# Kernel tuning notes

Measured on AMD Instinct MI355X. Metric: run time of the kernel, lower is better.

The kernel has to match this reference:

```python
import jax, jax.numpy as jnp
import numpy as np

N_NODES = 50000
N_EDGES = 800000


def _gcn_conv(x, src, dst, norm, W, b, num_nodes):
    # x: [N, Fin] -> h: [N, Fout]; messages gathered from src, scattered to dst.
    h = x @ W
    msgs = h[src] * norm[:, None]                      # [E+N, Fout]
    out = jax.ops.segment_sum(msgs, dst, num_segments=num_nodes)
    return out + b


def _gcn_norm(edge_index, num_nodes):
    # Add self-loops and compute symmetric normalization D^-1/2 (A+I) D^-1/2.
    loops = jnp.arange(num_nodes, dtype=edge_index.dtype)
    src = jnp.concatenate([edge_index[0], loops])
    dst = jnp.concatenate([edge_index[1], loops])
    ones = jnp.ones(src.shape[0], dtype=jnp.float32)
    deg = jax.ops.segment_sum(ones, dst, num_segments=num_nodes)
    dinv = jnp.where(deg > 0, jax.lax.rsqrt(jnp.maximum(deg, 1.0)), 0.0)
    norm = dinv[src] * dinv[dst]
    return src, dst, norm


def setup_inputs() -> dict:
    key = jax.random.key(0)
    k1, k2, k3, k4 = jax.random.split(key, 4)
    map_x = jax.random.normal(k1, (N_NODES, 128), dtype=jnp.float32)
    edge_index = jax.random.randint(k2, (2, N_EDGES), 0, N_NODES, dtype=jnp.int64)
    W1 = jax.random.normal(k3, (128, 64), dtype=jnp.float32) * (1.0 / np.sqrt(128))
    b1 = jnp.zeros((64,), dtype=jnp.float32)
    W2 = jax.random.normal(k4, (64, 32), dtype=jnp.float32) * (1.0 / np.sqrt(64))
    b2 = jnp.zeros((32,), dtype=jnp.float32)
    return {"map": map_x, "edge_index": edge_index, "W1": W1, "b1": b1, "W2": W2, "b2": b2}


def reference(map, edge_index, W1, b1, W2, b2):
    num_nodes = map.shape[0]
    src, dst, norm = _gcn_norm(edge_index, num_nodes)
    x = jax.nn.relu(_gcn_conv(map, src, dst, norm, W1, b1, num_nodes))
    x = jax.nn.relu(_gcn_conv(x, src, dst, norm, W2, b2, num_nodes))
    return x
```

## Files before the change

kernel.cpp:

```cpp
#include <hip/hip_runtime.h>

#define TPB 256
#define ACHUNK 4096
#define BSHIFT 6
#define BNODES 64
#define CAP 2048

__device__ __forceinline__ float blo(unsigned u) { return __uint_as_float(u << 16); }
__device__ __forceinline__ float bhi(unsigned u) { return __uint_as_float(u & 0xffff0000u); }
__device__ __forceinline__ unsigned pack2(float a, float b) {
    unsigned ua = __float_as_uint(a); ua += 0x7fffu + ((ua >> 16) & 1u);
    unsigned ub = __float_as_uint(b); ub += 0x7fffu + ((ub >> 16) & 1u);
    return (ua >> 16) | (ub & 0xffff0000u);
}
__device__ __forceinline__ void dec8(uint4 v, float* f) {
    f[0] = blo(v.x); f[1] = bhi(v.x); f[2] = blo(v.y); f[3] = bhi(v.y);
    f[4] = blo(v.z); f[5] = bhi(v.z); f[6] = blo(v.w); f[7] = bhi(v.w);
}
__device__ __forceinline__ void dec4(uint2 v, float* f) {
    f[0] = blo(v.x); f[1] = bhi(v.x); f[2] = blo(v.y); f[3] = bhi(v.y);
}


__global__ __launch_bounds__(TPB) void k_fat(
        const int* __restrict__ src, const int* __restrict__ dst, int E,
        int* __restrict__ bcnt, int* __restrict__ tmp, int NB,
        const float* __restrict__ X, const float* __restrict__ W,
        unsigned int* __restrict__ H1b, int N, int G1, int FB) {
    __shared__ float Ws[128 * 64];
    int* lcnt = (int*)Ws;
    int bid = blockIdx.x;
    int t = threadIdx.x;

    if ((bid % 5) == 0) {
        int fidx = bid / 5;
        if (fidx >= FB) return;
        int c0 = fidx * ACHUNK;
        int s_[16], d_[16];
#pragma unroll
        for (int i = 0; i < 16; i++) {
            int e = c0 + i * TPB + t;
            if (e < E) { s_[i] = src[e]; d_[i] = dst[e]; }
            else d_[i] = -1;
        }
        for (int b = t; b < NB; b += TPB) lcnt[b] = 0;
        __syncthreads();
#pragma unroll
        for (int i = 0; i < 16; i++)
            if (d_[i] >= 0) atomicAdd(&lcnt[d_[i] >> BSHIFT], 1);
        __syncthreads();
        for (int b = t; b < NB; b += TPB) {
            int c = lcnt[b];
            lcnt[b] = c ? (b * CAP + atomicAdd(&bcnt[b], c)) : 0;
        }
        __syncthreads();
#pragma unroll
        for (int i = 0; i < 16; i++) {
            if (d_[i] >= 0) {
                int bkt = d_[i] >> BSHIFT;
                int pos = atomicAdd(&lcnt[bkt], 1);
                if (pos < (bkt + 1) * CAP) {
                    tmp[pos] = ((d_[i] & (BNODES - 1)) << 16) | s_[i];
                }
            }
        }
    } else {
        int gb = bid - bid / 5 - 1;
        if (gb >= G1) return;
        int row0 = gb * 64;

        const float4* W4 = (const float4*)W;
        float4* Ws4 = (float4*)Ws;
#pragma unroll
        for (int i = 0; i < 8; i++) Ws4[t + i * 256] = W4[t + i * 256];
        __syncthreads();

        int r = t >> 2;
        int c0 = (t & 3) * 16;
        if (row0 + r >= N) return;
        const float4* xr = (const float4*)(X + (size_t)(row0 + r) * 128);
        float acc[16];
#pragma unroll
        for (int j = 0; j < 16; j++) acc[j] = 0.0f;
        for (int kk = 0; kk < 32; kk++) {
            float4 xv = xr[kk];
            const float* w0 = Ws + (4 * kk) * 64 + c0;
#pragma unroll
            for (int j = 0; j < 16; j++) acc[j] = fmaf(xv.x, w0[j], acc[j]);
#pragma unroll
            for (int j = 0; j < 16; j++) acc[j] = fmaf(xv.y, w0[64 + j], acc[j]);
#pragma unroll
            for (int j = 0; j < 16; j++) acc[j] = fmaf(xv.z, w0[128 + j], acc[j]);
#pragma unroll
            for (int j = 0; j < 16; j++) acc[j] = fmaf(xv.w, w0[192 + j], acc[j]);
        }
        unsigned int* ho = H1b + (size_t)(row0 + r) * 32 + (t & 3) * 8;
        uint4 p0 = { pack2(acc[0], acc[1]), pack2(acc[2], acc[3]),
                     pack2(acc[4], acc[5]), pack2(acc[6], acc[7]) };
        uint4 p1 = { pack2(acc[8], acc[9]), pack2(acc[10], acc[11]),
                     pack2(acc[12], acc[13]), pack2(acc[14], acc[15]) };
        *(uint4*)ho = p0;
        *(uint4*)(ho + 4) = p1;
    }
}


__global__ __launch_bounds__(TPB) void k_binB(
        const int* __restrict__ bcnt, const int* __restrict__ tmp,
        int* __restrict__ rowptr, unsigned short* __restrict__ rowlen,
        float* __restrict__ dinv, unsigned short* __restrict__ edges,
        unsigned short* __restrict__ order,
        const unsigned int* __restrict__ H1b, unsigned int* __restrict__ g1b,
        int N) {
    __shared__ int hist[BNODES];
    __shared__ int cur[BNODES];
    __shared__ int sh[BNODES];
    __shared__ int db[BNODES];
    __shared__ float dl[BNODES];
    int b = blockIdx.x;
    int t = threadIdx.x;
    int node0 = b << BSHIFT;
    int nn = N - node0; if (nn > BNODES) nn = BNODES;
    int cnt = bcnt[b]; if (cnt > CAP) cnt = CAP;
    const int tb = b * CAP;

    if (t < BNODES) hist[t] = 0;
    __syncthreads();
    for (int i = t; i < cnt; i += TPB) atomicAdd(&hist[tmp[tb + i] >> 16], 1);
    __syncthreads();
    if (t < BNODES) sh[t] = hist[t];
    __syncthreads();
    for (int o = 1; o < BNODES; o <<= 1) {
        int x = (t >= o && t < BNODES) ? sh[t - o] : 0;
        __syncthreads();
        if (t < BNODES) sh[t] += x;
        __syncthreads();
    }
    int v = 0;
    if (t < BNODES) {
        v = hist[t];
        int excl = sh[t] - v;
        cur[t] = excl;
        float dv = rsqrtf((float)(v + 1));
        dl[t] = dv;
        if (t < nn) {
            dinv[node0 + t] = dv;
            rowptr[node0 + t] = tb + excl;
            rowlen[node0 + t] = (unsigned short)v;
        }
    }
    int dcap = v > 63 ? 63 : v;
    if (t < BNODES) db[t] = 0;
    __syncthreads();
    if (t < nn) atomicAdd(&db[dcap], 1);
    __syncthreads();
    int dc = (t < BNODES) ? db[t] : 0;
    if (t < BNODES) sh[t] = dc;
    __syncthreads();
    for (int o = 1; o < BNODES; o <<= 1) {
        int x = (t >= o && t < BNODES) ? sh[t - o] : 0;
        __syncthreads();
        if (t < BNODES) sh[t] += x;
        __syncthreads();
    }
    if (t < BNODES) db[t] = sh[t] - dc;
    __syncthreads();
    if (t < nn) {
        int pos = atomicAdd(&db[dcap], 1);
        order[node0 + pos] = (unsigned short)(node0 + t);
    }
    __syncthreads();
    for (int i = t; i < cnt; i += TPB) {
        int p = tmp[tb + i];
        int pos = atomicAdd(&cur[p >> 16], 1);
        edges[tb + pos] = (unsigned short)(p & 0xffff);
    }
    const uint4* H4 = (const uint4*)H1b;
    uint4* G4 = (uint4*)g1b;
    for (int i = t; i < nn * 8; i += TPB) {
        int r = i >> 3, q = i & 7;
        float dv = dl[r];
        float f[8];
        uint4 hv = H4[(size_t)(node0 + r) * 8 + q];
        dec8(hv, f);
        uint4 p = { pack2(f[0] * dv, f[1] * dv), pack2(f[2] * dv, f[3] * dv),
                    pack2(f[4] * dv, f[5] * dv), pack2(f[6] * dv, f[7] * dv) };
        G4[(size_t)(node0 + r) * 8 + q] = p;
    }
}


__global__ __launch_bounds__(TPB) void k_gg(
        const int* __restrict__ rowptr, const unsigned short* __restrict__ rowlen,
        const unsigned short* __restrict__ edges, const unsigned short* __restrict__ order,
        const unsigned int* __restrict__ g1b,
        const float* __restrict__ dinv, const float* __restrict__ b1,
        const float* __restrict__ W2, unsigned int* __restrict__ g2b, int N) {
    __shared__ float W2s[64 * 32];
    __shared__ float rows[32 * 68];
    __shared__ float dl[32];
    __shared__ int nid[32];
    __shared__ int nst[32];
    __shared__ int nlen[32];
    int t = threadIdx.x;
    int node0 = blockIdx.x * 32;
    int nn = N - node0; if (nn > 32) nn = 32;
    if (nn <= 0) return;

    {
        const float4* W4 = (const float4*)W2;
        float4* Wd = (float4*)W2s;
        Wd[t] = W4[t]; Wd[t + 256] = W4[t + 256];
    }
    if (t < nn) {
        int ord = order[node0 + t];
        nid[t] = ord;
        dl[t] = dinv[ord];
        nst[t] = rowptr[ord];
        nlen[t] = rowlen[ord];
    }
    __syncthreads();

    const uint4* G4 = (const uint4*)g1b;
    int nl = t >> 3;
    int lane = t & 7;
    if (nl < nn) {
        int ord = nid[nl];
        float acc[8], f[8];
        uint4 sv = G4[(size_t)ord * 8 + lane];
        dec8(sv, acc);
        int base = nst[nl], deg = nlen[nl];
        int j = 0;
        for (; j + 7 < deg; j += 8) {
            int s0 = edges[base + j],     s1 = edges[base + j + 1];
            int s2 = edges[base + j + 2], s3 = edges[base + j + 3];
            int s4 = edges[base + j + 4], s5 = edges[base + j + 5];
            int s6 = edges[base + j + 6], s7 = edges[base + j + 7];
            uint4 r0 = G4[(size_t)s0 * 8 + lane];
            uint4 r1 = G4[(size_t)s1 * 8 + lane];
            uint4 r2 = G4[(size_t)s2 * 8 + lane];
            uint4 r3 = G4[(size_t)s3 * 8 + lane];
            uint4 r4 = G4[(size_t)s4 * 8 + lane];
            uint4 r5 = G4[(size_t)s5 * 8 + lane];
            uint4 r6 = G4[(size_t)s6 * 8 + lane];
            uint4 r7 = G4[(size_t)s7 * 8 + lane];
            dec8(r0, f);
#pragma unroll
            for (int k = 0; k < 8; k++) acc[k] += f[k];
            dec8(r1, f);
#pragma unroll
            for (int k = 0; k < 8; k++) acc[k] += f[k];
            dec8(r2, f);
#pragma unroll
            for (int k = 0; k < 8; k++) acc[k] += f[k];
            dec8(r3, f);
#pragma unroll
            for (int k = 0; k < 8; k++) acc[k] += f[k];
            dec8(r4, f);
#pragma unroll
            for (int k = 0; k < 8; k++) acc[k] += f[k];
            dec8(r5, f);
#pragma unroll
            for (int k = 0; k < 8; k++) acc[k] += f[k];
            dec8(r6, f);
#pragma unroll
            for (int k = 0; k < 8; k++) acc[k] += f[k];
            dec8(r7, f);
#pragma unroll
            for (int k = 0; k < 8; k++) acc[k] += f[k];
        }
        for (; j < deg; j++) {
            int s0 = edges[base + j];
            uint4 r0 = G4[(size_t)s0 * 8 + lane];
            dec8(r0, f);
#pragma unroll
            for (int k = 0; k < 8; k++) acc[k] += f[k];
        }
        float w0 = dl[nl];
        const float4* bb4 = (const float4*)(b1 + lane * 8);
        float4 ba = bb4[0], bc = bb4[1];
        float* rr = rows + nl * 68 + lane * 8;
        rr[0] = fmaxf(fmaf(acc[0], w0, ba.x), 0.0f);
        rr[1] = fmaxf(fmaf(acc[1], w0, ba.y), 0.0f);
        rr[2] = fmaxf(fmaf(acc[2], w0, ba.z), 0.0f);
        rr[3] = fmaxf(fmaf(acc[3], w0, ba.w), 0.0f);
        rr[4] = fmaxf(fmaf(acc[4], w0, bc.x), 0.0f);
        rr[5] = fmaxf(fmaf(acc[5], w0, bc.y), 0.0f);
        rr[6] = fmaxf(fmaf(acc[6], w0, bc.z), 0.0f);
        rr[7] = fmaxf(fmaf(acc[7], w0, bc.w), 0.0f);
    }
    __syncthreads();

    int n = t >> 3;
    int c = t & 7;
    if (n < nn) {
        const float* row = rows + n * 68;
        float a0 = 0.0f, a1 = 0.0f, a2 = 0.0f, a3 = 0.0f;
#pragma unroll 8
        for (int k = 0; k < 64; k++) {
            float rv = row[k];
            const float* w = W2s + k * 32 + 4 * c;
            a0 = fmaf(rv, w[0], a0); a1 = fmaf(rv, w[1], a1);
            a2 = fmaf(rv, w[2], a2); a3 = fmaf(rv, w[3], a3);
        }
        float dv = dl[n];
        uint2 p = { pack2(a0 * dv, a1 * dv), pack2(a2 * dv, a3 * dv) };
        ((uint2*)g2b)[(size_t)nid[n] * 8 + c] = p;
    }
}


__global__ __launch_bounds__(TPB) void k_g32(
        const int* __restrict__ rowptr, const unsigned short* __restrict__ rowlen,
        const unsigned short* __restrict__ edges, const unsigned short* __restrict__ order,
        const unsigned int* __restrict__ g2b,
        const float* __restrict__ dinv, const float* __restrict__ b2,
        float* __restrict__ out, int N) {
    __shared__ float dl[32];
    __shared__ int nid[32];
    __shared__ int nst[32];
    __shared__ int nlen[32];
    int t = threadIdx.x;
    int node0 = blockIdx.x * 32;
    int nn = N - node0; if (nn > 32) nn = 32;
    if (nn <= 0) return;
    if (t < nn) {
        int ord = order[node0 + t];
        nid[t] = ord;
        dl[t] = dinv[ord];
        nst[t] = rowptr[ord];
        nlen[t] = rowlen[ord];
    }
    __syncthreads();

    int nl = t >> 3;
    int lane = t & 7;
    if (nl >= nn) return;

    const uint2* G2 = (const uint2*)g2b;
    int ord = nid[nl];
    float acc[4], f[4];
    uint2 sv = G2[(size_t)ord * 8 + lane];
    dec4(sv, acc);
    int base = nst[nl], deg = nlen[nl];
    int j = 0;
    for (; j + 7 < deg; j += 8) {
        int s0 = edges[base + j],     s1 = edges[base + j + 1];
        int s2 = edges[base + j + 2], s3 = edges[base + j + 3];
        int s4 = edges[base + j + 4], s5 = edges[base + j + 5];
        int s6 = edges[base + j + 6], s7 = edges[base + j + 7];
        uint2 r0 = G2[(size_t)s0 * 8 + lane];
        uint2 r1 = G2[(size_t)s1 * 8 + lane];
        uint2 r2 = G2[(size_t)s2 * 8 + lane];
        uint2 r3 = G2[(size_t)s3 * 8 + lane];
        uint2 r4 = G2[(size_t)s4 * 8 + lane];
        uint2 r5 = G2[(size_t)s5 * 8 + lane];
        uint2 r6 = G2[(size_t)s6 * 8 + lane];
        uint2 r7 = G2[(size_t)s7 * 8 + lane];
        dec4(r0, f); acc[0] += f[0]; acc[1] += f[1]; acc[2] += f[2]; acc[3] += f[3];
        dec4(r1, f); acc[0] += f[0]; acc[1] += f[1]; acc[2] += f[2]; acc[3] += f[3];
        dec4(r2, f); acc[0] += f[0]; acc[1] += f[1]; acc[2] += f[2]; acc[3] += f[3];
        dec4(r3, f); acc[0] += f[0]; acc[1] += f[1]; acc[2] += f[2]; acc[3] += f[3];
        dec4(r4, f); acc[0] += f[0]; acc[1] += f[1]; acc[2] += f[2]; acc[3] += f[3];
        dec4(r5, f); acc[0] += f[0]; acc[1] += f[1]; acc[2] += f[2]; acc[3] += f[3];
        dec4(r6, f); acc[0] += f[0]; acc[1] += f[1]; acc[2] += f[2]; acc[3] += f[3];
        dec4(r7, f); acc[0] += f[0]; acc[1] += f[1]; acc[2] += f[2]; acc[3] += f[3];
    }
    for (; j < deg; j++) {
        int s0 = edges[base + j];
        uint2 r0 = G2[(size_t)s0 * 8 + lane];
        dec4(r0, f); acc[0] += f[0]; acc[1] += f[1]; acc[2] += f[2]; acc[3] += f[3];
    }
    float w0 = dl[nl];
    const float4* bb4 = (const float4*)(b2 + lane * 4);
    float4 ba = bb4[0];
    float4 o0 = { fmaxf(fmaf(acc[0], w0, ba.x), 0.0f),
                  fmaxf(fmaf(acc[1], w0, ba.y), 0.0f),
                  fmaxf(fmaf(acc[2], w0, ba.z), 0.0f),
                  fmaxf(fmaf(acc[3], w0, ba.w), 0.0f) };
    *(float4*)(out + (size_t)ord * 32 + lane * 4) = o0;
}

static inline int cdiv(int a, int b) { return (a + b - 1) / b; }
static inline char* alignup(char* p) { return (char*)(((uintptr_t)p + 255) & ~(uintptr_t)255); }

extern "C" void kernel_launch(void* const* d_in, const int* in_sizes, int n_in,
                              void* d_out, int out_size, void* d_ws, size_t ws_size,
                              hipStream_t stream) {
    const float* x  = (const float*)d_in[0];
    const int*   ei = (const int*)d_in[1];
    const float* W1 = (const float*)d_in[2];
    const float* b1 = (const float*)d_in[3];
    const float* W2 = (const float*)d_in[4];
    const float* b2 = (const float*)d_in[5];
    float* out = (float*)d_out;

    int N = in_sizes[0] / 128;
    int E = in_sizes[1] / 2;
    const int* src = ei;
    const int* dst = ei + E;

    int NB = cdiv(N, BNODES);

    char* p = (char*)d_ws;
    float* dinv  = (float*)p;            p = alignup(p + sizeof(float) * N);
    int* rowptr  = (int*)p;              p = alignup(p + sizeof(int) * N);
    unsigned short* rowlen = (unsigned short*)p;  p = alignup(p + sizeof(short) * N);
    unsigned short* order  = (unsigned short*)p;  p = alignup(p + sizeof(short) * N);
    int* bcnt    = (int*)p;              p = alignup(p + sizeof(int) * 1024);
    int* tmp     = (int*)p;              p = alignup(p + sizeof(int) * (size_t)NB * CAP);
    unsigned short* edges = (unsigned short*)p;   p = alignup(p + sizeof(short) * (size_t)NB * CAP);
    unsigned int* h1b = (unsigned int*)p; p = alignup(p + sizeof(short) * (size_t)N * 64);
    unsigned int* g1b = (unsigned int*)p; p = alignup(p + sizeof(short) * (size_t)N * 64);
    unsigned int* g2b = (unsigned int*)p; p = alignup(p + sizeof(short) * (size_t)N * 32);

    dim3 blk(TPB);
    int FB = cdiv(E, ACHUNK);
    int G1 = cdiv(N, 64);
    int fat = 1;
    while ((fat + 4) / 5 < FB || fat - (fat + 4) / 5 < G1) fat++;

    hipMemsetAsync(bcnt, 0, sizeof(int) * 1024, stream);
    k_fat<<<fat, blk, 0, stream>>>(src, dst, E, bcnt, tmp, NB,
                                   x, W1, h1b, N, G1, FB);
    k_binB<<<NB, blk, 0, stream>>>(bcnt, tmp, rowptr, rowlen, dinv,
                                   edges, order, h1b, g1b, N);
    k_gg<<<cdiv(N, 32), blk, 0, stream>>>(rowptr, rowlen, edges, order, g1b,
                                          dinv, b1, W2, g2b, N);
    k_g32<<<cdiv(N, 32), blk, 0, stream>>>(rowptr, rowlen, edges, order, g2b,
                                           dinv, b2, out, N);
}
```

Measured before the change: 154.5 us.

## Register-tile first GEMM, drop degree-sorted node order, widen gather unroll

The first-layer GEMM in the fused kernel now has each thread compute a 4-row by 8-column register tile over 128 rows per block, reusing shared-memory weight loads across rows. The block interleave ratio changes from 1:4 to 1:2. The per-bucket degree-sort that produced a node order permutation is removed, so the aggregation kernels process nodes in natural order and skip the indirection. The second-layer gather loop is unrolled to 16 outstanding loads. Dropping the sort removes a scan and extra syncs in the binning kernel, but gives up degree-balanced wavefronts in the gather kernels.

Measured after the change: 151.4 us (median of 3 runs). -2.0%, faster.

```diff
diff --git a/kernel.cpp b/kernel.cpp
--- a/kernel.cpp
+++ b/kernel.cpp
@@ -5,6 +5,7 @@
 #define BSHIFT 6
 #define BNODES 64
 #define CAP 2048
+#define GROWS 128
 
 __device__ __forceinline__ float blo(unsigned u) { return __uint_as_float(u << 16); }
 __device__ __forceinline__ float bhi(unsigned u) { return __uint_as_float(u & 0xffff0000u); }
@@ -32,8 +33,8 @@
     int bid = blockIdx.x;
     int t = threadIdx.x;
 
-    if ((bid % 5) == 0) {
-        int fidx = bid / 5;
+    if ((bid % 3) == 0) {
+        int fidx = bid / 3;
         if (fidx >= FB) return;
         int c0 = fidx * ACHUNK;
         int s_[16], d_[16];
@@ -65,9 +66,9 @@
             }
         }
     } else {
-        int gb = bid - bid / 5 - 1;
+        int gb = bid - bid / 3 - 1;
         if (gb >= G1) return;
-        int row0 = gb * 64;
+        int row0 = gb * GROWS;
 
         const float4* W4 = (const float4*)W;
         float4* Ws4 = (float4*)Ws;
@@ -75,32 +76,50 @@
         for (int i = 0; i < 8; i++) Ws4[t + i * 256] = W4[t + i * 256];
         __syncthreads();
 
-        int r = t >> 2;
-        int c0 = (t & 3) * 16;
-        if (row0 + r >= N) return;
-        const float4* xr = (const float4*)(X + (size_t)(row0 + r) * 128);
-        float acc[16];
-#pragma unroll
-        for (int j = 0; j < 16; j++) acc[j] = 0.0f;
+        int rg = t >> 3;
+        int c0 = (t & 7) * 8;
+        int r0 = row0 + rg * 4;
+        int ri[4];
+#pragma unroll
+        for (int i = 0; i < 4; i++) ri[i] = (r0 + i < N) ? (r0 + i) : (N - 1);
+
+        float acc[4][8];
+#pragma unroll
+        for (int i = 0; i < 4; i++)
+#pragma unroll
+            for (int j = 0; j < 8; j++) acc[i][j] = 0.0f;
+
+        const float4* X4 = (const float4*)X;
         for (int kk = 0; kk < 32; kk++) {
-            float4 xv = xr[kk];
-            const float* w0 = Ws + (4 * kk) * 64 + c0;
-#pragma unroll
-            for (int j = 0; j < 16; j++) acc[j] = fmaf(xv.x, w0[j], acc[j]);
-#pragma unroll
-            for (int j = 0; j < 16; j++) acc[j] = fmaf(xv.y, w0[64 + j], acc[j]);
-#pragma unroll
-            for (int j = 0; j < 16; j++) acc[j] = fmaf(xv.z, w0[128 + j], acc[j]);
-#pragma unroll
-            for (int j = 0; j < 16; j++) acc[j] = fmaf(xv.w, w0[192 + j], acc[j]);
-        }
-        unsigned int* ho = H1b + (size_t)(row0 + r) * 32 + (t & 3) * 8;
-        uint4 p0 = { pack2(acc[0], acc[1]), pack2(acc[2], acc[3]),
-                     pack2(acc[4], acc[5]), pack2(acc[6], acc[7]) };
-        uint4 p1 = { pack2(acc[8], acc[9]), pack2(acc[10], acc[11]),
-                     pack2(acc[12], acc[13]), pack2(acc[14], acc[15]) };
-        *(uint4*)ho = p0;
-        *(uint4*)(ho + 4) = p1;
+            float4 xv[4];
+#pragma unroll
+            for (int i = 0; i < 4; i++) xv[i] = X4[(size_t)ri[i] * 32 + kk];
+#pragma unroll
+            for (int q = 0; q < 4; q++) {
+                const float* w = Ws + (4 * kk + q) * 64 + c0;
+                float wq[8];
+#pragma unroll
+                for (int j = 0; j < 8; j++) wq[j] = w[j];
+                float xq[4];
+                xq[0] = q == 0 ? xv[0].x : q == 1 ? xv[0].y : q == 2 ? xv[0].z : xv[0].w;
+                xq[1] = q == 0 ? xv[1].x : q == 1 ? xv[1].y : q == 2 ? xv[1].z : xv[1].w;
+                xq[2] = q == 0 ? xv[2].x : q == 1 ? xv[2].y : q == 2 ? xv[2].z : xv[2].w;
+                xq[3] = q == 0 ? xv[3].x : q == 1 ? xv[3].y : q == 2 ? xv[3].z : xv[3].w;
+#pragma unroll
+                for (int i = 0; i < 4; i++)
+#pragma unroll
+                    for (int j = 0; j < 8; j++)
+                        acc[i][j] = fmaf(xq[i], wq[j], acc[i][j]);
+            }
+        }
+#pragma unroll
+        for (int i = 0; i < 4; i++) {
+            if (r0 + i < N) {
+                uint4 p = { pack2(acc[i][0], acc[i][1]), pack2(acc[i][2], acc[i][3]),
+                            pack2(acc[i][4], acc[i][5]), pack2(acc[i][6], acc[i][7]) };
+                *(uint4*)(H1b + (size_t)(r0 + i) * 32 + (t & 7) * 4) = p;
+            }
+        }
     }
 }
 
@@ -109,13 +128,11 @@
         const int* __restrict__ bcnt, const int* __restrict__ tmp,
         int* __restrict__ rowptr, unsigned short* __restrict__ rowlen,
         float* __restrict__ dinv, unsigned short* __restrict__ edges,
-        unsigned short* __restrict__ order,
         const unsigned int* __restrict__ H1b, unsigned int* __restrict__ g1b,
         int N) {
     __shared__ int hist[BNODES];
     __shared__ int cur[BNODES];
     __shared__ int sh[BNODES];
-    __shared__ int db[BNODES];
     __shared__ float dl[BNODES];
     int b = blockIdx.x;
     int t = threadIdx.x;
@@ -136,9 +153,8 @@
         if (t < BNODES) sh[t] += x;
         __syncthreads();
     }
-    int v = 0;
     if (t < BNODES) {
-        v = hist[t];
+        int v = hist[t];
         int excl = sh[t] - v;
         cur[t] = excl;
         float dv = rsqrtf((float)(v + 1));
@@ -148,26 +164,6 @@
             rowptr[node0 + t] = tb + excl;
             rowlen[node0 + t] = (unsigned short)v;
         }
-    }
-    int dcap = v > 63 ? 63 : v;
-    if (t < BNODES) db[t] = 0;
-    __syncthreads();
-    if (t < nn) atomicAdd(&db[dcap], 1);
-    __syncthreads();
-    int dc = (t < BNODES) ? db[t] : 0;
-    if (t < BNODES) sh[t] = dc;
-    __syncthreads();
-    for (int o = 1; o < BNODES; o <<= 1) {
-        int x = (t >= o && t < BNODES) ? sh[t - o] : 0;
-        __syncthreads();
-        if (t < BNODES) sh[t] += x;
-        __syncthreads();
-    }
-    if (t < BNODES) db[t] = sh[t] - dc;
-    __syncthreads();
-    if (t < nn) {
-        int pos = atomicAdd(&db[dcap], 1);
-        order[node0 + pos] = (unsigned short)(node0 + t);
     }
     __syncthreads();
     for (int i = t; i < cnt; i += TPB) {
@@ -192,14 +188,13 @@
 
 __global__ __launch_bounds__(TPB) void k_gg(
         const int* __restrict__ rowptr, const unsigned short* __restrict__ rowlen,
-        const unsigned short* __restrict__ edges, const unsigned short* __restrict__ order,
+        const unsigned short* __restrict__ edges,
         const unsigned int* __restrict__ g1b,
         const float* __restrict__ dinv, const float* __restrict__ b1,
         const float* __restrict__ W2, unsigned int* __restrict__ g2b, int N) {
     __shared__ float W2s[64 * 32];
     __shared__ float rows[32 * 68];
     __shared__ float dl[32];
-    __shared__ int nid[32];
     __shared__ int nst[32];
     __shared__ int nlen[32];
     int t = threadIdx.x;
@@ -213,11 +208,9 @@
         Wd[t] = W4[t]; Wd[t + 256] = W4[t + 256];
     }
     if (t < nn) {
-        int ord = order[node0 + t];
-        nid[t] = ord;
-        dl[t] = dinv[ord];
-        nst[t] = rowptr[ord];
-        nlen[t] = rowlen[ord];
+        dl[t] = dinv[node0 + t];
+        nst[t] = rowptr[node0 + t];
+        nlen[t] = rowlen[node0 + t];
     }
     __syncthreads();
 
@@ -225,53 +218,25 @@
     int nl = t >> 3;
     int lane = t & 7;
     if (nl < nn) {
-        int ord = nid[nl];
         float acc[8], f[8];
-        uint4 sv = G4[(size_t)ord * 8 + lane];
+        uint4 sv = G4[(size_t)(node0 + nl) * 8 + lane];
         dec8(sv, acc);
         int base = nst[nl], deg = nlen[nl];
         int j = 0;
         for (; j + 7 < deg; j += 8) {
-            int s0 = edges[base + j],     s1 = edges[base + j + 1];
-            int s2 = edges[base + j + 2], s3 = edges[base + j + 3];
-            int s4 = edges[base + j + 4], s5 = edges[base + j + 5];
-            int s6 = edges[base + j + 6], s7 = edges[base + j + 7];
-            uint4 r0 = G4[(size_t)s0 * 8 + lane];
-            uint4 r1 = G4[(size_t)s1 * 8 + lane];
-            uint4 r2 = G4[(size_t)s2 * 8 + lane];
-            uint4 r3 = G4[(size_t)s3 * 8 + lane];
-            uint4 r4 = G4[(size_t)s4 * 8 + lane];
-            uint4 r5 = G4[(size_t)s5 * 8 + lane];
-            uint4 r6 = G4[(size_t)s6 * 8 + lane];
-            uint4 r7 = G4[(size_t)s7 * 8 + lane];
-            dec8(r0, f);
-#pragma unroll
-            for (int k = 0; k < 8; k++) acc[k] += f[k];
-            dec8(r1, f);
-#pragma unroll
-            for (int k = 0; k < 8; k++) acc[k] += f[k];
-            dec8(r2, f);
-#pragma unroll
-            for (int k = 0; k < 8; k++) acc[k] += f[k];
-            dec8(r3, f);
-#pragma unroll
-            for (int k = 0; k < 8; k++) acc[k] += f[k];
-            dec8(r4, f);
-#pragma unroll
-            for (int k = 0; k < 8; k++) acc[k] += f[k];
-            dec8(r5, f);
-#pragma unroll
-            for (int k = 0; k < 8; k++) acc[k] += f[k];
-            dec8(r6, f);
-#pragma unroll
-            for (int k = 0; k < 8; k++) acc[k] += f[k];
-            dec8(r7, f);
-#pragma unroll
-            for (int k = 0; k < 8; k++) acc[k] += f[k];
+            uint4 r[8];
+#pragma unroll
+            for (int u = 0; u < 8; u++)
+                r[u] = G4[(size_t)edges[base + j + u] * 8 + lane];
+#pragma unroll
+            for (int u = 0; u < 8; u++) {
+                dec8(r[u], f);
+#pragma unroll
+                for (int k = 0; k < 8; k++) acc[k] += f[k];
+            }
         }
         for (; j < deg; j++) {
-            int s0 = edges[base + j];
-            uint4 r0 = G4[(size_t)s0 * 8 + lane];
+            uint4 r0 = G4[(size_t)edges[base + j] * 8 + lane];
             dec8(r0, f);
 #pragma unroll
             for (int k = 0; k < 8; k++) acc[k] += f[k];
@@ -305,19 +270,18 @@
         }
         float dv = dl[n];
         uint2 p = { pack2(a0 * dv, a1 * dv), pack2(a2 * dv, a3 * dv) };
-        ((uint2*)g2b)[(size_t)nid[n] * 8 + c] = p;
+        ((uint2*)g2b)[(size_t)(node0 + n) * 8 + c] = p;
     }
 }
 
 
 __global__ __launch_bounds__(TPB) void k_g32(
         const int* __restrict__ rowptr, const unsigned short* __restrict__ rowlen,
-        const unsigned short* __restrict__ edges, const unsigned short* __restrict__ order,
+        const unsigned short* __restrict__ edges,
         const unsigned int* __restrict__ g2b,
         const float* __restrict__ dinv, const float* __restrict__ b2,
         float* __restrict__ out, int N) {
     __shared__ float dl[32];
-    __shared__ int nid[32];
     __shared__ int nst[32];
     __shared__ int nlen[32];
     int t = threadIdx.x;
@@ -325,11 +289,9 @@
     int nn = N - node0; if (nn > 32) nn = 32;
     if (nn <= 0) return;
     if (t < nn) {
-        int ord = order[node0 + t];
-        nid[t] = ord;
-        dl[t] = dinv[ord];
-        nst[t] = rowptr[ord];
-        nlen[t] = rowlen[ord];
+        dl[t] = dinv[node0 + t];
+        nst[t] = rowptr[node0 + t];
+        nlen[t] = rowlen[node0 + t];
     }
     __syncthreads();
 
@@ -338,38 +300,26 @@
     if (nl >= nn) return;
 
     const uint2* G2 = (const uint2*)g2b;
-    int ord = nid[nl];
     float acc[4], f[4];
-    uint2 sv = G2[(size_t)ord * 8 + lane];
+    uint2 sv = G2[(size_t)(node0 + nl) * 8 + lane];
     dec4(sv, acc);
     int base = nst[nl], deg = nlen[nl];
     int j = 0;
-    for (; j + 7 < deg; j += 8) {
-        int s0 = edges[base + j],     s1 = edges[base + j + 1];
-        int s2 = edges[base + j + 2], s3 = edges[base + j + 3];
-        int s4 = edges[base + j + 4], s5 = edges[base + j + 5];
-        int s6 = edges[base + j + 6], s7 = edges[base + j + 7];
-        uint2 r0 = G2[(size_t)s0 * 8 + lane];
-        uint2 r1 = G2[(size_t)s1 * 8 + lane];
-        uint2 r2 = G2[(size_t)s2 * 8 + lane];
-        uint2 r3 = G2[(size_t)s3 * 8 + lane];
-        uint2 r4 = G2[(size_t)s4 * 8 + lane];
-        uint2 r5 = G2[(size_t)s5 * 8 + lane];
-        uint2 r6 = G2[(size_t)s6 * 8 + lane];
-        uint2 r7 = G2[(size_t)s7 * 8 + lane];
-        dec4(r0, f); acc[0] += f[0]; acc[1] += f[1]; acc[2] += f[2]; acc[3] += f[3];
-        dec4(r1, f); acc[0] += f[0]; acc[1] += f[1]; acc[2] += f[2]; acc[3] += f[3];
-        dec4(r2, f); acc[0] += f[0]; acc[1] += f[1]; acc[2] += f[2]; acc[3] += f[3];
-        dec4(r3, f); acc[0] += f[0]; acc[1] += f[1]; acc[2] += f[2]; acc[3] += f[3];
-        dec4(r4, f); acc[0] += f[0]; acc[1] += f[1]; acc[2] += f[2]; acc[3] += f[3];
-        dec4(r5, f); acc[0] += f[0]; acc[1] += f[1]; acc[2] += f[2]; acc[3] += f[3];
-        dec4(r6, f); acc[0] += f[0]; acc[1] += f[1]; acc[2] += f[2]; acc[3] += f[3];
-        dec4(r7, f); acc[0] += f[0]; acc[1] += f[1]; acc[2] += f[2]; acc[3] += f[3];
+    for (; j + 15 < deg; j += 16) {
+        uint2 r[16];
+#pragma unroll
+        for (int u = 0; u < 16; u++)
+            r[u] = G2[(size_t)edges[base + j + u] * 8 + lane];
+#pragma unroll
+        for (int u = 0; u < 16; u++) {
+            dec4(r[u], f);
+            acc[0] += f[0]; acc[1] += f[1]; acc[2] += f[2]; acc[3] += f[3];
+        }
     }
     for (; j < deg; j++) {
-        int s0 = edges[base + j];
-        uint2 r0 = G2[(size_t)s0 * 8 + lane];
-        dec4(r0, f); acc[0] += f[0]; acc[1] += f[1]; acc[2] += f[2]; acc[3] += f[3];
+        uint2 r0 = G2[(size_t)edges[base + j] * 8 + lane];
+        dec4(r0, f);
+        acc[0] += f[0]; acc[1] += f[1]; acc[2] += f[2]; acc[3] += f[3];
     }
     float w0 = dl[nl];
     const float4* bb4 = (const float4*)(b2 + lane * 4);
@@ -378,7 +328,7 @@
                   fmaxf(fmaf(acc[1], w0, ba.y), 0.0f),
                   fmaxf(fmaf(acc[2], w0, ba.z), 0.0f),
                   fmaxf(fmaf(acc[3], w0, ba.w), 0.0f) };
-    *(float4*)(out + (size_t)ord * 32 + lane * 4) = o0;
+    *(float4*)(out + (size_t)(node0 + nl) * 32 + lane * 4) = o0;
 }
 
 static inline int cdiv(int a, int b) { return (a + b - 1) / b; }
@@ -406,7 +356,6 @@
     float* dinv  = (float*)p;            p = alignup(p + sizeof(float) * N);
     int* rowptr  = (int*)p;              p = alignup(p + sizeof(int) * N);
     unsigned short* rowlen = (unsigned short*)p;  p = alignup(p + sizeof(short) * N);
-    unsigned short* order  = (unsigned short*)p;  p = alignup(p + sizeof(short) * N);
     int* bcnt    = (int*)p;              p = alignup(p + sizeof(int) * 1024);
     int* tmp     = (int*)p;              p = alignup(p + sizeof(int) * (size_t)NB * CAP);
     unsigned short* edges = (unsigned short*)p;   p = alignup(p + sizeof(short) * (size_t)NB * CAP);
@@ -416,17 +365,17 @@
 
     dim3 blk(TPB);
     int FB = cdiv(E, ACHUNK);
-    int G1 = cdiv(N, 64);
+    int G1 = cdiv(N, GROWS);
     int fat = 1;
-    while ((fat + 4) / 5 < FB || fat - (fat + 4) / 5 < G1) fat++;
+    while ((fat + 2) / 3 < FB || fat - (fat + 2) / 3 < G1) fat++;
 
     hipMemsetAsync(bcnt, 0, sizeof(int) * 1024, stream);
     k_fat<<<fat, blk, 0, stream>>>(src, dst, E, bcnt, tmp, NB,
                                    x, W1, h1b, N, G1, FB);
     k_binB<<<NB, blk, 0, stream>>>(bcnt, tmp, rowptr, rowlen, dinv,
-                                   edges, order, h1b, g1b, N);
-    k_gg<<<cdiv(N, 32), blk, 0, stream>>>(rowptr, rowlen, edges, order, g1b,
+                                   edges, h1b, g1b, N);
+    k_gg<<<cdiv(N, 32), blk, 0, stream>>>(rowptr, rowlen, edges, g1b,
                                           dinv, b1, W2, g2b, N);
-    k_g32<<<cdiv(N, 32), blk, 0, stream>>>(rowptr, rowlen, edges, order, g2b,
+    k_g32<<<cdiv(N, 32), blk, 0, stream>>>(rowptr, rowlen, edges, g2b,
                                            dinv, b2, out, N);
 }
```
